# Kernel optimization log

Hardware: AMD Instinct MI355X
Metric: run time of the kernel (lower is better)

The kernel has to match this reference:

```python
import jax, jax.numpy as jnp
import numpy as np

EPS = 1e-7
T_NCE = 0.07      # opt.nce_t
MOMENTUM = 0.5    # opt.nce_m
N_DATA = 100000   # opt.n_data


def l2norm(x):
    # Normalize(power=2): x / (sum(x^2, dim=1))^(1/2)
    return x / jnp.sqrt(jnp.sum(x * x, axis=1, keepdims=True))


def contrast_loss(x, P):
    # ContrastLoss (Eq 18). x: [B, P+K] of normalized exp-similarities.
    B, PK = x.shape
    N = PK - P
    m_pn = N * (1.0 / N_DATA)  # m * Pn
    pos = x[:, :P]                                   # [B, P]
    log_D1 = jnp.log(pos / (pos + m_pn + EPS))
    neg = x[:, P:]                                   # [B, N]
    log_D0 = jnp.log(m_pn / (neg + m_pn + EPS))
    # log_D0.view(-1,1).repeat(1,P).sum(0) == P copies of log_D0.sum()
    return -((log_D1.sum(0) + log_D0.sum()) / B).sum() / P


def setup_inputs() -> dict:
    key = jax.random.key(0)
    ks = jax.random.split(key, 10)
    B, S_DIM, T_DIM, FEAT = 64, 2048, 2048, 128
    P, K = 4, 8192
    NCLS, PER = 7, 1000
    stdv = 1.0 / np.sqrt(FEAT / 3.0)
    return {
        "f_s": jax.random.normal(ks[0], (B, S_DIM), jnp.float32),
        "f_t": jax.random.normal(ks[1], (B, T_DIM), jnp.float32),
        "idx": jax.random.randint(ks[2], (B,), 0, N_DATA),
        "batch_label": jax.random.uniform(ks[3], (B, NCLS), dtype=jnp.float32),
        "class_index": jax.random.randint(ks[4], (NCLS, PER), 0, N_DATA),
        "num_pos": P,
        "contrast_idx": jax.random.randint(ks[5], (B, P + K), 0, N_DATA),
        "W_s": jax.random.normal(ks[6], (S_DIM, FEAT), jnp.float32) * 0.02,
        "b_s": jnp.zeros((FEAT,), jnp.float32),
        "W_t": jax.random.normal(ks[7], (T_DIM, FEAT), jnp.float32) * 0.02,
        "b_t": jnp.zeros((FEAT,), jnp.float32),
        "memory_s": jax.random.uniform(ks[8], (N_DATA, FEAT), jnp.float32, -stdv, stdv),
        "memory_t": jax.random.uniform(ks[9], (N_DATA, FEAT), jnp.float32, -stdv, stdv),
    }


def reference(f_s, f_t, idx, batch_label, class_index, num_pos, contrast_idx,
              W_s, b_s, W_t, b_t, memory_s, memory_t):
    # Embed + L2 norm
    f_s = l2norm(f_s @ W_s + b_s)   # [B, D]
    f_t = l2norm(f_t @ W_t + b_t)   # [B, D]

    # ContrastMemory (memory banks are buffers -> no grad through them)
    mem_s = jax.lax.stop_gradient(memory_s)
    mem_t = jax.lax.stop_gradient(memory_t)

    w_t = mem_t[contrast_idx]                                     # [B, P+K, D]
    out_s = jnp.exp(jnp.einsum('bkd,bd->bk', w_t, f_s) / T_NCE)
    out_s = out_s / (jnp.mean(out_s) * N_DATA)                    # Z_s normalization
    w_s = mem_s[contrast_idx]                                     # [B, P+K, D]
    out_t = jnp.exp(jnp.einsum('bkd,bd->bk', w_s, f_t) / T_NCE)
    out_t = out_t / (jnp.mean(out_t) * N_DATA)                    # Z_t normalization

    # momentum memory update (done under no_grad in torch)
    upd_s = l2norm(mem_s[idx] * MOMENTUM + jax.lax.stop_gradient(f_s) * (1.0 - MOMENTUM))
    new_mem_s = mem_s.at[idx].set(upd_s)
    upd_t = l2norm(mem_t[idx] * MOMENTUM + jax.lax.stop_gradient(f_t) * (1.0 - MOMENTUM))
    new_mem_t = mem_t.at[idx].set(upd_t)

    CCD_loss = contrast_loss(out_s, num_pos) + contrast_loss(out_t, num_pos)

    # class-center anchors: gather per-class memory rows, relu, mean -> [NCLS, D]
    s_anchors = l2norm(jnp.mean(jax.nn.relu(new_mem_s[class_index]), axis=1))
    t_anchors = l2norm(jnp.mean(jax.nn.relu(new_mem_t[class_index]), axis=1))

    # anchor relation loss (anchors detached; teacher relation fully detached)
    s_rel = (f_s @ jax.lax.stop_gradient(s_anchors).T) / T_NCE    # [B, NCLS]
    t_rel = jax.lax.stop_gradient((f_t @ t_anchors.T) / T_NCE)
    targets = jax.nn.softmax(t_rel, axis=1)
    log_inputs = jax.nn.log_softmax(s_rel, axis=1)
    relation_loss = jnp.sum(targets * (jnp.log(targets + EPS * 0 + 1e-30) - log_inputs)) / s_rel.shape[0]

    return (CCD_loss, relation_loss, f_s, f_t)
```

## Files before the change

kernel.cpp:

```cpp
#include <hip/hip_runtime.h>
#include <math.h>
#include <stdint.h>

#define B 64
#define SDIM 2048
#define FEAT 128
#define P 4
#define PK 8196
#define NCLS 7
#define PER 1000
#define NDATA 100000
#define EPSC 1e-7f
#define M_PN 0.08192f
#define JCHUNKS 50
#define CS (PER / JCHUNKS)

#define DTSZ (64 * NDATA)
#define KSPLIT 4
#define KSEG 2049
#define KS1 8
#define TPW 4
#define ROWS_BLK (4 * TPW * 16)

#define TILE 16
#define WCHUNK 512
#define NT (WCHUNK / TILE)

#define GLL16(gp, lp) \
    __builtin_amdgcn_global_load_lds( \
        (__attribute__((address_space(1))) void*)(uintptr_t)(gp), \
        (__attribute__((address_space(3))) void*)(lp), 16, 0, 0)

typedef __attribute__((ext_vector_type(8))) short bf16x8;
typedef __attribute__((ext_vector_type(4))) float f32x4;

static __device__ __forceinline__ short f2bf(float x)
{
    union { float f; uint32_t u; } v; v.f = x;
    const uint32_t r = (v.u + 0x7fffu + ((v.u >> 16) & 1u)) >> 16;
    return (short)r;
}

__global__ void gemm_partial_kernel(const float* __restrict__ f_s,
                                    const float* __restrict__ f_t,
                                    const float* __restrict__ W_s,
                                    const float* __restrict__ W_t,
                                    float* __restrict__ fb)
{
    const int row = blockIdx.x;
    const int z   = blockIdx.y;
    const int ks  = blockIdx.z;
    const float* f = z == 0 ? f_s : f_t;
    const float* W = z == 0 ? W_s : W_t;

    const int t  = threadIdx.x;
    const int d  = t & 127;
    const int kh = t >> 7;

    __shared__ float frow[SDIM / KS1];
    frow[t] = f[row * SDIM + ks * (SDIM / KS1) + t];
    __syncthreads();

    float acc = 0.0f;
    const int kb = ks * (SDIM / KS1) + kh * 128;
    #pragma unroll 8
    for (int k = 0; k < 128; ++k)
        acc = fmaf(frow[kh * 128 + k], W[(kb + k) * FEAT + d], acc);

    __shared__ float part[2][128];
    part[kh][d] = acc;
    __syncthreads();
    if (t < 128)
        atomicAdd(&fb[((size_t)z * B + row) * FEAT + t], part[0][t] + part[1][t]);
}

__global__ void norm_finish_kernel(const float* __restrict__ fb,
                                   const float* __restrict__ b_s,
                                   const float* __restrict__ b_t,
                                   float* __restrict__ out_fs,
                                   float* __restrict__ out_ft,
                                   unsigned short* __restrict__ fsb,
                                   unsigned short* __restrict__ ftb)
{
    const int row = blockIdx.x;
    const int z   = blockIdx.y;
    const int d   = threadIdx.x;
    const float* bias = z == 0 ? b_s : b_t;
    float* out = z == 0 ? out_fs : out_ft;
    unsigned short* fbx = z == 0 ? fsb : ftb;

    const float a = fb[((size_t)z * B + row) * FEAT + d] + bias[d];
    __shared__ float red[128];
    red[d] = a * a;
    __syncthreads();
    for (int s = 64; s > 0; s >>= 1) {
        if (d < s) red[d] += red[d + s];
        __syncthreads();
    }
    const float v = a * (1.0f / sqrtf(red[0]));
    out[row * FEAT + d] = v;
    fbx[row * FEAT + d] = (unsigned short)f2bf(v);
}

#define MFMA4(av, kc, a0, a1, a2, a3) do { \
    a0 = __builtin_amdgcn_mfma_f32_16x16x32_bf16(av, bv[kc][0], a0, 0, 0, 0); \
    a1 = __builtin_amdgcn_mfma_f32_16x16x32_bf16(av, bv[kc][1], a1, 0, 0, 0); \
    a2 = __builtin_amdgcn_mfma_f32_16x16x32_bf16(av, bv[kc][2], a2, 0, 0, 0); \
    a3 = __builtin_amdgcn_mfma_f32_16x16x32_bf16(av, bv[kc][3], a3, 0, 0, 0); \
    } while (0)

__global__ __launch_bounds__(256, 2)
void dgemm6_kernel(const unsigned short* __restrict__ fsb,
                   const unsigned short* __restrict__ ftb,
                   const float* __restrict__ mem_s,
                   const float* __restrict__ mem_t,
                   float* __restrict__ DT0,
                   float* __restrict__ DT1,
                   int zbase)
{
    const int z = blockIdx.y + zbase;
    const unsigned short* fWb = z == 0 ? fsb : ftb;
    const float* mem          = z == 0 ? mem_t : mem_s;
    float* DT                 = z == 0 ? DT0 : DT1;

    const int tid = threadIdx.x;
    const int w   = tid >> 6;
    const int l   = tid & 63;
    const int ln  = l & 15;
    const int ko  = l >> 4;
    const int xk  = ln & 7;
    const int wrowbase = blockIdx.x * ROWS_BLK + w * (TPW * 16);

    __shared__ __align__(16) float rows[4][2][16 * FEAT];

    bf16x8 bv[4][4];
    #pragma unroll
    for (int kc = 0; kc < 4; ++kc)
        #pragma unroll
        for (int nt = 0; nt < 4; ++nt)
            bv[kc][nt] = *(const bf16x8*)(fWb + (nt * 16 + ln) * FEAT + kc * 32 + ko * 8);

#define STG(tt, bf) do { \
    _Pragma("unroll") \
    for (int p_ = 0; p_ < 8; ++p_) { \
        const int r_ = 2 * p_ + (l >> 5); \
        int gr_ = wrowbase + (tt) * 16 + r_; \
        if (gr_ >= NDATA) gr_ = NDATA - 1; \
        const float* g_ = mem + (size_t)gr_ * FEAT + (((l & 31) ^ (r_ & 7)) << 2); \
        GLL16(g_, &rows[w][bf][p_ * 256]); \
    } } while (0)

    STG(0, 0);
    int cur = 0;
    #pragma unroll
    for (int t = 0; t < TPW; ++t) {
        if (t + 1 < TPW) {
            STG(t + 1, cur ^ 1);
            if (t == 0) {
                asm volatile("s_waitcnt vmcnt(8)" ::: "memory");
            } else {
                asm volatile("s_waitcnt vmcnt(12)" ::: "memory");
            }
        } else {
            asm volatile("s_waitcnt vmcnt(4)" ::: "memory");
        }
        __builtin_amdgcn_sched_barrier(0);

        const float* rb = &rows[w][cur][ln * FEAT];
        f32x4 c0 = (f32x4){0.f,0.f,0.f,0.f};
        f32x4 c1 = (f32x4){0.f,0.f,0.f,0.f};
        f32x4 c2 = (f32x4){0.f,0.f,0.f,0.f};
        f32x4 c3 = (f32x4){0.f,0.f,0.f,0.f};
        #pragma unroll
        for (int kc = 0; kc < 4; ++kc) {
            const int g0 = kc * 8 + ko * 2;
            const float4 lo = *(const float4*)(rb + (((g0 + 0) ^ xk) << 2));
            const float4 hi = *(const float4*)(rb + (((g0 + 1) ^ xk) << 2));
            const bf16x8 av = (bf16x8){ f2bf(lo.x), f2bf(lo.y), f2bf(lo.z), f2bf(lo.w),
                                        f2bf(hi.x), f2bf(hi.y), f2bf(hi.z), f2bf(hi.w) };
            MFMA4(av, kc, c0, c1, c2, c3);
        }

        const int growb = wrowbase + t * 16 + ko * 4;
        if (growb < NDATA) {
            *(f32x4*)(DT + (size_t)( 0 + ln) * NDATA + growb) = c0;
            *(f32x4*)(DT + (size_t)(16 + ln) * NDATA + growb) = c1;
            *(f32x4*)(DT + (size_t)(32 + ln) * NDATA + growb) = c2;
            *(f32x4*)(DT + (size_t)(48 + ln) * NDATA + growb) = c3;
        }
        cur ^= 1;
    }
#undef STG
}

__global__ void gather2_kernel(const int* __restrict__ contrast_idx,
                               const float* __restrict__ DT0,
                               const float* __restrict__ DT1,
                               float* __restrict__ out_raw,
                               float* __restrict__ Ssum)
{
    const int z   = blockIdx.z;
    const int b   = blockIdx.y;
    const int ks  = blockIdx.x;
    const int tid = threadIdx.x;
    const int k0  = ks * KSEG;
    const int kend = min(k0 + KSEG, PK);
    const float inv_t = 1.0f / 0.07f;
    const float* dtb = (z == 0 ? DT0 : DT1) + (size_t)b * NDATA;
    float* orz = out_raw + (size_t)z * (B * PK);
    float lsum = 0.0f;
    #pragma unroll 4
    for (int k = k0 + tid; k < kend; k += 256) {
        const int ci = contrast_idx[(size_t)b * PK + k];
        const float v = expf(dtb[ci] * inv_t);
        orz[(size_t)b * PK + k] = v;
        lsum += v;
    }
    __shared__ float red[256];
    red[tid] = lsum;
    __syncthreads();
    for (int s = 128; s > 0; s >>= 1) {
        if (tid < s) red[tid] += red[tid + s];
        __syncthreads();
    }
    if (tid == 0) atomicAdd(&Ssum[z], red[0]);
}

__global__ void ccd_loss_kernel(const float* __restrict__ out_raw,
                                const float* __restrict__ Ssum,
                                float* __restrict__ acc)
{
    const int z = blockIdx.y;
    const float S = Ssum[z];
    const float c = ((float)(B * PK)) / (S * (float)NDATA);

    const int total = B * PK;
    float contrib = 0.0f;
    for (int i = blockIdx.x * blockDim.x + threadIdx.x; i < total;
         i += gridDim.x * blockDim.x) {
        const float v = out_raw[(size_t)z * total + i] * c;
        const int k = i % PK;
        if (k < P) {
            contrib += logf(v / (v + M_PN + EPSC));
        } else {
            contrib += (float)P * logf(M_PN / (v + M_PN + EPSC));
        }
    }
    __shared__ float red[256];
    red[threadIdx.x] = contrib;
    __syncthreads();
    for (int s = 128; s > 0; s >>= 1) {
        if (threadIdx.x < s) red[threadIdx.x] += red[threadIdx.x + s];
        __syncthreads();
    }
    if (threadIdx.x == 0) atomicAdd(&acc[z], red[0]);
}

__global__ void gemm_norm_kernel(const float* __restrict__ f_s,
                                 const float* __restrict__ f_t,
                                 const float* __restrict__ W_s,
                                 const float* __restrict__ b_s,
                                 const float* __restrict__ W_t,
                                 const float* __restrict__ b_t,
                                 float* __restrict__ out_fs,
                                 float* __restrict__ out_ft)
{
    const int row = blockIdx.x;
    const int z   = blockIdx.y;
    const float* f    = z == 0 ? f_s : f_t;
    const float* W    = z == 0 ? W_s : W_t;
    const float* bias = z == 0 ? b_s : b_t;
    float* out        = z == 0 ? out_fs : out_ft;

    __shared__ __align__(16) float frow[SDIM];
    const int t  = threadIdx.x;
    const int d  = t & 127;
    const int kh = t >> 7;
    for (int k = t; k < SDIM; k += 256) frow[k] = f[row * SDIM + k];
    __syncthreads();

    float acc = 0.0f;
    const int k0 = kh * (SDIM / 2);
    for (int k = k0; k < k0 + SDIM / 2; ++k)
        acc = fmaf(frow[k], W[k * FEAT + d], acc);

    __shared__ float part[2][128];
    part[kh][d] = acc;
    __syncthreads();
    const float a = part[0][d] + part[1][d] + bias[d];

    __shared__ float red[256];
    red[t] = (t < 128) ? a * a : 0.0f;
    __syncthreads();
    for (int s = 128; s > 0; s >>= 1) {
        if (t < s) red[t] += red[t + s];
        __syncthreads();
    }
    if (t < 128) out[row * FEAT + t] = a * (1.0f / sqrtf(red[0]));
}

__global__ __launch_bounds__(64)
void dots_kernel(const float* __restrict__ fsn,
                 const float* __restrict__ ftn,
                 const int*   __restrict__ contrast_idx,
                 const float* __restrict__ mem_s,
                 const float* __restrict__ mem_t,
                 float* __restrict__ out_raw,
                 float* __restrict__ Ssum)
{
    const int z = blockIdx.z;
    const int b = blockIdx.y;
    const int l = threadIdx.x;
    const int kchunk = blockIdx.x * WCHUNK;

    const float* f   = (z == 0 ? fsn : ftn) + b * FEAT;
    const float* mem = (z == 0 ? mem_t : mem_s);

    __shared__ __align__(16) float rows[2][TILE * FEAT];
    __shared__ __align__(16) float fl[FEAT];
    __shared__ int cis[WCHUNK];

    fl[l]      = f[l];
    fl[l + 64] = f[l + 64];
    for (int i = l; i < WCHUNK; i += 64) {
        const int k = kchunk + i;
        cis[i] = contrast_idx[(size_t)b * PK + (k < PK ? k : PK - 1)];
    }
    __syncthreads();

    const int q   = l >> 4;
    const int r_c = l & 15;
    const int xk  = r_c & 7;
    const int rh  = l >> 5;
    const int sl  = l & 31;

    const float4* fg = (const float4*)fl;
    const float4 f0 = fg[q * 8 + 0], f1 = fg[q * 8 + 1];
    const float4 f2 = fg[q * 8 + 2], f3 = fg[q * 8 + 3];
    const float4 f4 = fg[q * 8 + 4], f5 = fg[q * 8 + 5];
    const float4 f6 = fg[q * 8 + 6], f7 = fg[q * 8 + 7];

    const float inv_t = 1.0f / 0.07f;
    const size_t obase = (size_t)z * (B * PK) + (size_t)b * PK;
    float lsum = 0.0f;

#define STAGE(tt, bf) do { \
    _Pragma("unroll") \
    for (int p_ = 0; p_ < 8; ++p_) { \
        const int rr_ = 2 * p_ + rh; \
        const int ci_ = cis[(tt) * TILE + rr_]; \
        const float* g_ = mem + (size_t)ci_ * FEAT + ((sl ^ (rr_ & 7)) << 2); \
        GLL16(g_, &rows[bf][p_ * 256]); \
    } } while (0)

    STAGE(0, 0);
    int cur = 0;
    for (int t = 0; t < NT; ++t) {
        if (t + 1 < NT) {
            STAGE(t + 1, cur ^ 1);
            asm volatile("s_waitcnt vmcnt(8)" ::: "memory");
        } else {
            asm volatile("s_waitcnt vmcnt(0)" ::: "memory");
        }
        __builtin_amdgcn_sched_barrier(0);

        const float* rbase = &rows[cur][r_c * FEAT];
        float dot;
        {
            const float4 m0 = *(const float4*)(rbase + (((q * 8 + 0) ^ xk) << 2));
            const float4 m1 = *(const float4*)(rbase + (((q * 8 + 1) ^ xk) << 2));
            const float4 m2 = *(const float4*)(rbase + (((q * 8 + 2) ^ xk) << 2));
            const float4 m3 = *(const float4*)(rbase + (((q * 8 + 3) ^ xk) << 2));
            const float4 m4 = *(const float4*)(rbase + (((q * 8 + 4) ^ xk) << 2));
            const float4 m5 = *(const float4*)(rbase + (((q * 8 + 5) ^ xk) << 2));
            const float4 m6 = *(const float4*)(rbase + (((q * 8 + 6) ^ xk) << 2));
            const float4 m7 = *(const float4*)(rbase + (((q * 8 + 7) ^ xk) << 2));
            dot = m0.x * f0.x;
            dot = fmaf(m0.y, f0.y, dot); dot = fmaf(m0.z, f0.z, dot); dot = fmaf(m0.w, f0.w, dot);
            dot = fmaf(m1.x, f1.x, dot); dot = fmaf(m1.y, f1.y, dot); dot = fmaf(m1.z, f1.z, dot); dot = fmaf(m1.w, f1.w, dot);
            dot = fmaf(m2.x, f2.x, dot); dot = fmaf(m2.y, f2.y, dot); dot = fmaf(m2.z, f2.z, dot); dot = fmaf(m2.w, f2.w, dot);
            dot = fmaf(m3.x, f3.x, dot); dot = fmaf(m3.y, f3.y, dot); dot = fmaf(m3.z, f3.z, dot); dot = fmaf(m3.w, f3.w, dot);
            dot = fmaf(m4.x, f4.x, dot); dot = fmaf(m4.y, f4.y, dot); dot = fmaf(m4.z, f4.z, dot); dot = fmaf(m4.w, f4.w, dot);
            dot = fmaf(m5.x, f5.x, dot); dot = fmaf(m5.y, f5.y, dot); dot = fmaf(m5.z, f5.z, dot); dot = fmaf(m5.w, f5.w, dot);
            dot = fmaf(m6.x, f6.x, dot); dot = fmaf(m6.y, f6.y, dot); dot = fmaf(m6.z, f6.z, dot); dot = fmaf(m6.w, f6.w, dot);
            dot = fmaf(m7.x, f7.x, dot); dot = fmaf(m7.y, f7.y, dot); dot = fmaf(m7.z, f7.z, dot); dot = fmaf(m7.w, f7.w, dot);
        }
        dot += __shfl_xor(dot, 16);
        dot += __shfl_xor(dot, 32);

        const int krow = kchunk + t * TILE + r_c;
        if (q == 0 && krow < PK) {
            const float val = expf(dot * inv_t);
            out_raw[obase + krow] = val;
            lsum += val;
        }
        cur ^= 1;
    }
#undef STAGE

    lsum += __shfl_xor(lsum, 8);
    lsum += __shfl_xor(lsum, 4);
    lsum += __shfl_xor(lsum, 2);
    lsum += __shfl_xor(lsum, 1);
    if (l == 0) atomicAdd(&Ssum[z], lsum);
}

__global__ void upd_kernel(const float* __restrict__ fsn,
                           const float* __restrict__ ftn,
                           const int*   __restrict__ idx,
                           const float* __restrict__ mem_s,
                           const float* __restrict__ mem_t,
                           float* __restrict__ upd)
{
    const int z = blockIdx.y;
    const int b = blockIdx.x;
    const int d = threadIdx.x;
    const float* mem = z == 0 ? mem_s : mem_t;
    const float* f   = z == 0 ? fsn : ftn;
    const int i = idx[b];
    const float v = mem[(size_t)i * FEAT + d] * 0.5f + f[b * FEAT + d] * 0.5f;
    __shared__ float red[128];
    red[d] = v * v;
    __syncthreads();
    for (int s = 64; s > 0; s >>= 1) {
        if (d < s) red[d] += red[d + s];
        __syncthreads();
    }
    upd[(size_t)z * (B * FEAT) + b * FEAT + d] = v * (1.0f / sqrtf(red[0]));
}

__global__ void remap_kernel(const int* __restrict__ class_index,
                             const int* __restrict__ idx,
                             int* __restrict__ remap)
{
    const int e = blockIdx.x * 256 + threadIdx.x;
    if (e >= NCLS * PER) return;
    const int ci = class_index[e];
    int rb = -1;
    for (int b = B - 1; b >= 0; --b) {
        if (idx[b] == ci) { rb = b; break; }
    }
    remap[e] = rb;
}

__global__ void anchors_partial_kernel(const int* __restrict__ class_index,
                                       const int* __restrict__ remap,
                                       const float* __restrict__ mem_s,
                                       const float* __restrict__ mem_t,
                                       const float* __restrict__ upd,
                                       float* __restrict__ partial)
{
    const int z     = blockIdx.z;
    const int c     = blockIdx.y;
    const int chunk = blockIdx.x;
    const int d     = threadIdx.x;
    const float* mem = z == 0 ? mem_s : mem_t;
    const float* u   = upd + (size_t)z * (B * FEAT);
    float acc = 0.0f;
    #pragma unroll 4
    for (int j = chunk * CS; j < chunk * CS + CS; ++j) {
        const int e = c * PER + j;
        const int ci = class_index[e];
        const int rb = remap[e];
        const float* row = (rb >= 0) ? (u + rb * FEAT) : (mem + (size_t)ci * FEAT);
        const float v = row[d];
        acc += v > 0.0f ? v : 0.0f;
    }
    atomicAdd(&partial[(size_t)z * (NCLS * FEAT) + c * FEAT + d], acc);
}

__global__ void anchors_finish_kernel(const float* __restrict__ partial,
                                      float* __restrict__ anchors)
{
    const int z = blockIdx.y;
    const int c = blockIdx.x;
    const int d = threadIdx.x;
    const float meanv = partial[(size_t)z * (NCLS * FEAT) + c * FEAT + d]
                        * (1.0f / (float)PER);
    __shared__ float red[128];
    red[d] = meanv * meanv;
    __syncthreads();
    for (int s = 64; s > 0; s >>= 1) {
        if (d < s) red[d] += red[d + s];
        __syncthreads();
    }
    anchors[(size_t)z * (NCLS * FEAT) + c * FEAT + d] = meanv * (1.0f / sqrtf(red[0]));
}

__global__ void final_kernel(const float* __restrict__ fsn,
                             const float* __restrict__ ftn,
                             const float* __restrict__ anchors,
                             const float* __restrict__ acc,
                             float* __restrict__ d_out)
{
    __shared__ float sa[NCLS * FEAT];
    __shared__ float ta[NCLS * FEAT];
    const int tid = threadIdx.x;
    for (int i = tid; i < NCLS * FEAT; i += 64) {
        sa[i] = anchors[i];
        ta[i] = anchors[NCLS * FEAT + i];
    }
    __syncthreads();

    const int b = tid;
    float srel[NCLS], trel[NCLS];
    for (int j = 0; j < NCLS; ++j) { srel[j] = 0.0f; trel[j] = 0.0f; }
    for (int d = 0; d < FEAT; ++d) {
        const float fs = fsn[b * FEAT + d];
        const float ft = ftn[b * FEAT + d];
        #pragma unroll
        for (int j = 0; j < NCLS; ++j) {
            srel[j] = fmaf(fs, sa[j * FEAT + d], srel[j]);
            trel[j] = fmaf(ft, ta[j * FEAT + d], trel[j]);
        }
    }
    const float inv_t = 1.0f / 0.07f;
    float smax = -1e30f, tmax = -1e30f;
    for (int j = 0; j < NCLS; ++j) {
        srel[j] *= inv_t; trel[j] *= inv_t;
        smax = fmaxf(smax, srel[j]);
        tmax = fmaxf(tmax, trel[j]);
    }
    float ssum = 0.0f, tsum = 0.0f;
    float texp[NCLS];
    for (int j = 0; j < NCLS; ++j) {
        ssum += expf(srel[j] - smax);
        texp[j] = expf(trel[j] - tmax);
        tsum += texp[j];
    }
    const float lse_s = logf(ssum);
    float contrib = 0.0f;
    for (int j = 0; j < NCLS; ++j) {
        const float tgt = texp[j] / tsum;
        const float log_in = srel[j] - smax - lse_s;
        contrib += tgt * (logf(tgt + 1e-30f) - log_in);
    }
    for (int off = 32; off > 0; off >>= 1) contrib += __shfl_down(contrib, off);
    if (tid == 0) {
        d_out[1] = contrib / (float)B;
        d_out[0] = -(acc[0] + acc[1]) / (float)(B * P);
    }
}

extern "C" void kernel_launch(void* const* d_in, const int* in_sizes, int n_in,
                              void* d_out_v, int out_size, void* d_ws, size_t ws_size,
                              hipStream_t stream)
{
    const float* f_s = (const float*)d_in[0];
    const float* f_t = (const float*)d_in[1];
    const int*   idx = (const int*)d_in[2];
    const int*   class_index = (const int*)d_in[4];
    const int*   contrast_idx = (const int*)d_in[6];
    const float* W_s = (const float*)d_in[7];
    const float* b_s = (const float*)d_in[8];
    const float* W_t = (const float*)d_in[9];
    const float* b_t = (const float*)d_in[10];
    const float* mem_s = (const float*)d_in[11];
    const float* mem_t = (const float*)d_in[12];

    float* out    = (float*)d_out_v;
    float* out_fs = out + 2;
    float* out_ft = out + 2 + B * FEAT;

    float* ws = (float*)d_ws;
    const size_t fl = ws_size / sizeof(float);
    const size_t REST = 2 * (size_t)B * PK
                      + (size_t)B * FEAT
                      + 2 * B * FEAT
                      + 2 * B * FEAT
                      + 4 * NCLS * FEAT
                      + NCLS * PER
                      + 64;
    const bool big   = fl >= 2 * (size_t)DTSZ + REST;
    const bool small = fl >= 1 * (size_t)DTSZ + REST;

    if (small) {
        float* DT0 = ws;
        float* DT1 = big ? ws + DTSZ : DT0;
        float* p   = (big ? ws + 2 * (size_t)DTSZ : ws + DTSZ);
        float* out_raw = p;            p += 2 * (size_t)B * PK;
        unsigned short* fsb = (unsigned short*)p;  p += B * FEAT / 2;
        unsigned short* ftb = (unsigned short*)p;  p += B * FEAT / 2;
        float* fb      = p;            p += 2 * B * FEAT;
        float* partial = p;            p += 2 * NCLS * FEAT;
        float* Ssum    = p;            p += 2;
        float* acc     = p;            p += 2;
        float* upd     = p;            p += 2 * B * FEAT;
        float* anchors = p;            p += 2 * NCLS * FEAT;
        int*   remap   = (int*)p;

        hipMemsetAsync(fb, 0,
                       (2 * B * FEAT + 2 * NCLS * FEAT + 4) * sizeof(float),
                       stream);

        dim3 g1a(B, 2, KS1);
        gemm_partial_kernel<<<g1a, 256, 0, stream>>>(f_s, f_t, W_s, W_t, fb);
        dim3 g1b(B, 2);
        norm_finish_kernel<<<g1b, 128, 0, stream>>>(fb, b_s, b_t,
                                                    out_fs, out_ft, fsb, ftb);

        const int gblocks = (NDATA + ROWS_BLK - 1) / ROWS_BLK;
        if (big) {
            dim3 gd(gblocks, 2);
            dgemm6_kernel<<<gd, 256, 0, stream>>>(fsb, ftb, mem_s, mem_t,
                                                  DT0, DT1, 0);
            dim3 gg(KSPLIT, B, 2);
            gather2_kernel<<<gg, 256, 0, stream>>>(contrast_idx, DT0, DT1,
                                                   out_raw, Ssum);
        } else {
            dim3 gd(gblocks, 1);
            dim3 gg(KSPLIT, B, 1);
            dgemm6_kernel<<<gd, 256, 0, stream>>>(fsb, ftb, mem_s, mem_t,
                                                  DT0, DT0, 0);
            gather2_kernel<<<gg, 256, 0, stream>>>(contrast_idx, DT0, DT0,
                                                   out_raw, Ssum);
            dgemm6_kernel<<<gd, 256, 0, stream>>>(fsb, ftb, mem_s, mem_t,
                                                  DT0, DT0, 1);
            gather2_kernel<<<gg, 256, 0, stream>>>(contrast_idx, DT0, DT0,
                                                   out_raw + (size_t)B * PK,
                                                   Ssum + 1);
        }

        dim3 g3(256, 2);
        ccd_loss_kernel<<<g3, 256, 0, stream>>>(out_raw, Ssum, acc);
        dim3 g4(B, 2);
        upd_kernel<<<g4, 128, 0, stream>>>(out_fs, out_ft, idx, mem_s, mem_t, upd);
        remap_kernel<<<(NCLS * PER + 255) / 256, 256, 0, stream>>>(class_index, idx, remap);
        dim3 g5a(JCHUNKS, NCLS, 2);
        anchors_partial_kernel<<<g5a, 128, 0, stream>>>(class_index, remap,
                                                        mem_s, mem_t, upd, partial);
        dim3 g5b(NCLS, 2);
        anchors_finish_kernel<<<g5b, 128, 0, stream>>>(partial, anchors);
        final_kernel<<<1, 64, 0, stream>>>(out_fs, out_ft, anchors, acc, out);
    } else {
        float* out_raw = ws;
        float* upd     = out_raw + 2 * (B * PK);
        float* anchors = upd + 2 * (B * FEAT);
        float* partial = anchors + 2 * (NCLS * FEAT);
        float* Ssum    = partial + 2 * (NCLS * FEAT);
        float* acc     = Ssum + 2;
        int*   remap   = (int*)(acc + 2);

        hipMemsetAsync(partial, 0, (2 * NCLS * FEAT + 4) * sizeof(float), stream);

        dim3 g1(B, 2);
        gemm_norm_kernel<<<g1, 256, 0, stream>>>(f_s, f_t, W_s, b_s, W_t, b_t,
                                                 out_fs, out_ft);
        dim3 g2((PK + WCHUNK - 1) / WCHUNK, B, 2);
        dots_kernel<<<g2, 64, 0, stream>>>(out_fs, out_ft, contrast_idx,
                                           mem_s, mem_t, out_raw, Ssum);
        dim3 g3(256, 2);
        ccd_loss_kernel<<<g3, 256, 0, stream>>>(out_raw, Ssum, acc);
        dim3 g4(B, 2);
        upd_kernel<<<g4, 128, 0, stream>>>(out_fs, out_ft, idx, mem_s, mem_t, upd);
        remap_kernel<<<(NCLS * PER + 255) / 256, 256, 0, stream>>>(class_index, idx, remap);
        dim3 g5a(JCHUNKS, NCLS, 2);
        anchors_partial_kernel<<<g5a, 128, 0, stream>>>(class_index, remap,
                                                        mem_s, mem_t, upd, partial);
        dim3 g5b(NCLS, 2);
        anchors_finish_kernel<<<g5b, 128, 0, stream>>>(partial, anchors);
        final_kernel<<<1, 64, 0, stream>>>(out_fs, out_ft, anchors, acc, out);
    }
}
```

Baseline: 117.6 us.

## Fuse small tail kernels and replace atomic GEMM split-K with partial buffers

```diff
diff --git a/kernel.cpp b/kernel.cpp
--- a/kernel.cpp
+++ b/kernel.cpp
@@ -45,7 +45,7 @@
                                     const float* __restrict__ f_t,
                                     const float* __restrict__ W_s,
                                     const float* __restrict__ W_t,
-                                    float* __restrict__ fb)
+                                    float* __restrict__ fbp)
 {
     const int row = blockIdx.x;
     const int z   = blockIdx.y;
@@ -71,16 +71,20 @@
     part[kh][d] = acc;
     __syncthreads();
     if (t < 128)
-        atomicAdd(&fb[((size_t)z * B + row) * FEAT + t], part[0][t] + part[1][t]);
-}
-
-__global__ void norm_finish_kernel(const float* __restrict__ fb,
+        fbp[(((size_t)ks * 2 + z) * B + row) * FEAT + t] = part[0][t] + part[1][t];
+}
+
+__global__ void norm_finish_kernel(const float* __restrict__ fbp,
                                    const float* __restrict__ b_s,
                                    const float* __restrict__ b_t,
+                                   const int*   __restrict__ idx,
+                                   const float* __restrict__ mem_s,
+                                   const float* __restrict__ mem_t,
                                    float* __restrict__ out_fs,
                                    float* __restrict__ out_ft,
                                    unsigned short* __restrict__ fsb,
-                                   unsigned short* __restrict__ ftb)
+                                   unsigned short* __restrict__ ftb,
+                                   float* __restrict__ upd)
 {
     const int row = blockIdx.x;
     const int z   = blockIdx.y;
@@ -89,7 +93,11 @@
     float* out = z == 0 ? out_fs : out_ft;
     unsigned short* fbx = z == 0 ? fsb : ftb;
 
-    const float a = fb[((size_t)z * B + row) * FEAT + d] + bias[d];
+    float a = bias[d];
+    #pragma unroll
+    for (int ks = 0; ks < KS1; ++ks)
+        a += fbp[(((size_t)ks * 2 + z) * B + row) * FEAT + d];
+
     __shared__ float red[128];
     red[d] = a * a;
     __syncthreads();
@@ -100,6 +108,18 @@
     const float v = a * (1.0f / sqrtf(red[0]));
     out[row * FEAT + d] = v;
     fbx[row * FEAT + d] = (unsigned short)f2bf(v);
+    __syncthreads();
+
+    const float* mem = z == 0 ? mem_s : mem_t;
+    const int i = idx[row];
+    const float u = mem[(size_t)i * FEAT + d] * 0.5f + v * 0.5f;
+    red[d] = u * u;
+    __syncthreads();
+    for (int s = 64; s > 0; s >>= 1) {
+        if (d < s) red[d] += red[d + s];
+        __syncthreads();
+    }
+    upd[((size_t)z * B + row) * FEAT + d] = u * (1.0f / sqrtf(red[0]));
 }
 
 #define MFMA4(av, kc, a0, a1, a2, a3) do { \
@@ -429,26 +449,12 @@
     upd[(size_t)z * (B * FEAT) + b * FEAT + d] = v * (1.0f / sqrtf(red[0]));
 }
 
-__global__ void remap_kernel(const int* __restrict__ class_index,
-                             const int* __restrict__ idx,
-                             int* __restrict__ remap)
-{
-    const int e = blockIdx.x * 256 + threadIdx.x;
-    if (e >= NCLS * PER) return;
-    const int ci = class_index[e];
-    int rb = -1;
-    for (int b = B - 1; b >= 0; --b) {
-        if (idx[b] == ci) { rb = b; break; }
-    }
-    remap[e] = rb;
-}
-
-__global__ void anchors_partial_kernel(const int* __restrict__ class_index,
-                                       const int* __restrict__ remap,
-                                       const float* __restrict__ mem_s,
-                                       const float* __restrict__ mem_t,
-                                       const float* __restrict__ upd,
-                                       float* __restrict__ partial)
+__global__ void anchors_partial2_kernel(const int* __restrict__ class_index,
+                                        const int* __restrict__ idx,
+                                        const float* __restrict__ mem_s,
+                                        const float* __restrict__ mem_t,
+                                        const float* __restrict__ upd,
+                                        float* __restrict__ partial)
 {
     const int z     = blockIdx.z;
     const int c     = blockIdx.y;
@@ -456,12 +462,29 @@
     const int d     = threadIdx.x;
     const float* mem = z == 0 ? mem_s : mem_t;
     const float* u   = upd + (size_t)z * (B * FEAT);
+
+    __shared__ int lidx[B];
+    __shared__ int cis[CS];
+    __shared__ int rbs[CS];
+    if (d < B) lidx[d] = idx[d];
+    __syncthreads();
+    if (d < CS) {
+        const int e = c * PER + chunk * CS + d;
+        const int ci = class_index[e];
+        int rb = -1;
+        for (int b = B - 1; b >= 0; --b) {
+            if (lidx[b] == ci) { rb = b; break; }
+        }
+        cis[d] = ci;
+        rbs[d] = rb;
+    }
+    __syncthreads();
+
     float acc = 0.0f;
     #pragma unroll 4
-    for (int j = chunk * CS; j < chunk * CS + CS; ++j) {
-        const int e = c * PER + j;
-        const int ci = class_index[e];
-        const int rb = remap[e];
+    for (int j = 0; j < CS; ++j) {
+        const int ci = cis[j];
+        const int rb = rbs[j];
         const float* row = (rb >= 0) ? (u + rb * FEAT) : (mem + (size_t)ci * FEAT);
         const float v = row[d];
         acc += v > 0.0f ? v : 0.0f;
@@ -469,76 +492,69 @@
     atomicAdd(&partial[(size_t)z * (NCLS * FEAT) + c * FEAT + d], acc);
 }
 
-__global__ void anchors_finish_kernel(const float* __restrict__ partial,
-                                      float* __restrict__ anchors)
-{
-    const int z = blockIdx.y;
-    const int c = blockIdx.x;
-    const int d = threadIdx.x;
-    const float meanv = partial[(size_t)z * (NCLS * FEAT) + c * FEAT + d]
-                        * (1.0f / (float)PER);
+__global__ void final2_kernel(const float* __restrict__ fsn,
+                              const float* __restrict__ ftn,
+                              const float* __restrict__ partial,
+                              const float* __restrict__ acc,
+                              float* __restrict__ d_out)
+{
+    __shared__ float an[2 * NCLS * FEAT];
     __shared__ float red[128];
-    red[d] = meanv * meanv;
-    __syncthreads();
-    for (int s = 64; s > 0; s >>= 1) {
-        if (d < s) red[d] += red[d + s];
-        __syncthreads();
-    }
-    anchors[(size_t)z * (NCLS * FEAT) + c * FEAT + d] = meanv * (1.0f / sqrtf(red[0]));
-}
-
-__global__ void final_kernel(const float* __restrict__ fsn,
-                             const float* __restrict__ ftn,
-                             const float* __restrict__ anchors,
-                             const float* __restrict__ acc,
-                             float* __restrict__ d_out)
-{
-    __shared__ float sa[NCLS * FEAT];
-    __shared__ float ta[NCLS * FEAT];
     const int tid = threadIdx.x;
-    for (int i = tid; i < NCLS * FEAT; i += 64) {
-        sa[i] = anchors[i];
-        ta[i] = anchors[NCLS * FEAT + i];
-    }
-    __syncthreads();
-
-    const int b = tid;
-    float srel[NCLS], trel[NCLS];
-    for (int j = 0; j < NCLS; ++j) { srel[j] = 0.0f; trel[j] = 0.0f; }
-    for (int d = 0; d < FEAT; ++d) {
-        const float fs = fsn[b * FEAT + d];
-        const float ft = ftn[b * FEAT + d];
-        #pragma unroll
+
+    for (int zc = 0; zc < 2 * NCLS; ++zc) {
+        const float mv = partial[(size_t)zc * FEAT + tid] * (1.0f / (float)PER);
+        red[tid] = mv * mv;
+        __syncthreads();
+        for (int s = 64; s > 0; s >>= 1) {
+            if (tid < s) red[tid] += red[tid + s];
+            __syncthreads();
+        }
+        an[zc * FEAT + tid] = mv * (1.0f / sqrtf(red[0]));
+        __syncthreads();
+    }
+
+    float contrib = 0.0f;
+    if (tid < 64) {
+        const int b = tid;
+        const float* sa = an;
+        const float* ta = an + NCLS * FEAT;
+        float srel[NCLS], trel[NCLS];
+        for (int j = 0; j < NCLS; ++j) { srel[j] = 0.0f; trel[j] = 0.0f; }
+        for (int d = 0; d < FEAT; ++d) {
+            const float fs = fsn[b * FEAT + d];
+            const float ft = ftn[b * FEAT + d];
+            #pragma unroll
+            for (int j = 0; j < NCLS; ++j) {
+                srel[j] = fmaf(fs, sa[j * FEAT + d], srel[j]);
+                trel[j] = fmaf(ft, ta[j * FEAT + d], trel[j]);
+            }
+        }
+        const float inv_t = 1.0f / 0.07f;
+        float smax = -1e30f, tmax = -1e30f;
         for (int j = 0; j < NCLS; ++j) {
-            srel[j] = fmaf(fs, sa[j * FEAT + d], srel[j]);
-            trel[j] = fmaf(ft, ta[j * FEAT + d], trel[j]);
-        }
-    }
-    const float inv_t = 1.0f / 0.07f;
-    float smax = -1e30f, tmax = -1e30f;
-    for (int j = 0; j < NCLS; ++j) {
-        srel[j] *= inv_t; trel[j] *= inv_t;
-        smax = fmaxf(smax, srel[j]);
-        tmax = fmaxf(tmax, trel[j]);
-    }
-    float ssum = 0.0f, tsum = 0.0f;
-    float texp[NCLS];
-    for (int j = 0; j < NCLS; ++j) {
-        ssum += expf(srel[j] - smax);
-        texp[j] = expf(trel[j] - tmax);
-        tsum += texp[j];
-    }
-    const float lse_s = logf(ssum);
-    float contrib = 0.0f;
-    for (int j = 0; j < NCLS; ++j) {
-        const float tgt = texp[j] / tsum;
-        const float log_in = srel[j] - smax - lse_s;
-        contrib += tgt * (logf(tgt + 1e-30f) - log_in);
-    }
-    for (int off = 32; off > 0; off >>= 1) contrib += __shfl_down(contrib, off);
-    if (tid == 0) {
-        d_out[1] = contrib / (float)B;
-        d_out[0] = -(acc[0] + acc[1]) / (float)(B * P);
+            srel[j] *= inv_t; trel[j] *= inv_t;
+            smax = fmaxf(smax, srel[j]);
+            tmax = fmaxf(tmax, trel[j]);
+        }
+        float ssum = 0.0f, tsum = 0.0f;
+        float texp[NCLS];
+        for (int j = 0; j < NCLS; ++j) {
+            ssum += expf(srel[j] - smax);
+            texp[j] = expf(trel[j] - tmax);
+            tsum += texp[j];
+        }
+        const float lse_s = logf(ssum);
+        for (int j = 0; j < NCLS; ++j) {
+            const float tgt = texp[j] / tsum;
+            const float log_in = srel[j] - smax - lse_s;
+            contrib += tgt * (logf(tgt + 1e-30f) - log_in);
+        }
+        for (int off = 32; off > 0; off >>= 1) contrib += __shfl_down(contrib, off);
+        if (tid == 0) {
+            d_out[1] = contrib / (float)B;
+            d_out[0] = -(acc[0] + acc[1]) / (float)(B * P);
+        }
     }
 }
 
@@ -566,10 +582,9 @@
     const size_t fl = ws_size / sizeof(float);
     const size_t REST = 2 * (size_t)B * PK
                       + (size_t)B * FEAT
+                      + (size_t)KS1 * 2 * B * FEAT
                       + 2 * B * FEAT
-                      + 2 * B * FEAT
-                      + 4 * NCLS * FEAT
-                      + NCLS * PER
+                      + 2 * NCLS * FEAT
                       + 64;
     const bool big   = fl >= 2 * (size_t)DTSZ + REST;
     const bool small = fl >= 1 * (size_t)DTSZ + REST;
@@ -581,23 +596,20 @@
         float* out_raw = p;            p += 2 * (size_t)B * PK;
         unsigned short* fsb = (unsigned short*)p;  p += B * FEAT / 2;
         unsigned short* ftb = (unsigned short*)p;  p += B * FEAT / 2;
-        float* fb      = p;            p += 2 * B * FEAT;
+        float* fbp     = p;            p += (size_t)KS1 * 2 * B * FEAT;
+        float* upd     = p;            p += 2 * B * FEAT;
         float* partial = p;            p += 2 * NCLS * FEAT;
         float* Ssum    = p;            p += 2;
         float* acc     = p;            p += 2;
-        float* upd     = p;            p += 2 * B * FEAT;
-        float* anchors = p;            p += 2 * NCLS * FEAT;
-        int*   remap   = (int*)p;
-
-        hipMemsetAsync(fb, 0,
-                       (2 * B * FEAT + 2 * NCLS * FEAT + 4) * sizeof(float),
-                       stream);
+
+        hipMemsetAsync(partial, 0, (2 * NCLS * FEAT + 4) * sizeof(float), stream);
 
         dim3 g1a(B, 2, KS1);
-        gemm_partial_kernel<<<g1a, 256, 0, stream>>>(f_s, f_t, W_s, W_t, fb);
+        gemm_partial_kernel<<<g1a, 256, 0, stream>>>(f_s, f_t, W_s, W_t, fbp);
         dim3 g1b(B, 2);
-        norm_finish_kernel<<<g1b, 128, 0, stream>>>(fb, b_s, b_t,
-                                                    out_fs, out_ft, fsb, ftb);
+        norm_finish_kernel<<<g1b, 128, 0, stream>>>(fbp, b_s, b_t, idx,
+                                                    mem_s, mem_t,
+                                                    out_fs, out_ft, fsb, ftb, upd);
 
         const int gblocks = (NDATA + ROWS_BLK - 1) / ROWS_BLK;
         if (big) {
@@ -623,23 +635,16 @@
 
         dim3 g3(256, 2);
         ccd_loss_kernel<<<g3, 256, 0, stream>>>(out_raw, Ssum, acc);
-        dim3 g4(B, 2);
-        upd_kernel<<<g4, 128, 0, stream>>>(out_fs, out_ft, idx, mem_s, mem_t, upd);
-        remap_kernel<<<(NCLS * PER + 255) / 256, 256, 0, stream>>>(class_index, idx, remap);
         dim3 g5a(JCHUNKS, NCLS, 2);
-        anchors_partial_kernel<<<g5a, 128, 0, stream>>>(class_index, remap,
-                                                        mem_s, mem_t, upd, partial);
-        dim3 g5b(NCLS, 2);
-        anchors_finish_kernel<<<g5b, 128, 0, stream>>>(partial, anchors);
-        final_kernel<<<1, 64, 0, stream>>>(out_fs, out_ft, anchors, acc, out);
+        anchors_partial2_kernel<<<g5a, 128, 0, stream>>>(class_index, idx,
+                                                         mem_s, mem_t, upd, partial);
+        final2_kernel<<<1, 128, 0, stream>>>(out_fs, out_ft, partial, acc, out);
     } else {
         float* out_raw = ws;
         float* upd     = out_raw + 2 * (B * PK);
-        float* anchors = upd + 2 * (B * FEAT);
-        float* partial = anchors + 2 * (NCLS * FEAT);
+        float* partial = upd + 2 * (B * FEAT);
         float* Ssum    = partial + 2 * (NCLS * FEAT);
         float* acc     = Ssum + 2;
-        int*   remap   = (int*)(acc + 2);
 
         hipMemsetAsync(partial, 0, (2 * NCLS * FEAT + 4) * sizeof(float), stream);
 
@@ -653,12 +658,9 @@
         ccd_loss_kernel<<<g3, 256, 0, stream>>>(out_raw, Ssum, acc);
         dim3 g4(B, 2);
         upd_kernel<<<g4, 128, 0, stream>>>(out_fs, out_ft, idx, mem_s, mem_t, upd);
-        remap_kernel<<<(NCLS * PER + 255) / 256, 256, 0, stream>>>(class_index, idx, remap);
         dim3 g5a(JCHUNKS, NCLS, 2);
-        anchors_partial_kernel<<<g5a, 128, 0, stream>>>(class_index, remap,
-                                                        mem_s, mem_t, upd, partial);
-        dim3 g5b(NCLS, 2);
-        anchors_finish_kernel<<<g5b, 128, 0, stream>>>(partial, anchors);
-        final_kernel<<<1, 64, 0, stream>>>(out_fs, out_ft, anchors, acc, out);
-    }
-}
+        anchors_partial2_kernel<<<g5a, 128, 0, stream>>>(class_index, idx,
+                                                         mem_s, mem_t, upd, partial);
+        final2_kernel<<<1, 128, 0, stream>>>(out_fs, out_ft, partial, acc, out);
+    }
+}
```

Result: slower. 120.0 us (+2.1%).
